# Optimization experiments

Hardware: AMD Instinct MI355X
Metric: run time of the kernel (lower is better)

The kernel has to match this reference:

```python
import jax, jax.numpy as jnp
import numpy as np

B, N, D, H = 4, 2048, 1024, 16
HD = D // H
SCALE = D ** -0.5  # NOTE: original scales by dimension**-0.5 (not head_dim**-0.5)


def setup_inputs() -> dict:
    key = jax.random.key(0)
    k1, k2, k3 = jax.random.split(key, 3)
    x = jax.random.normal(k1, (B, N, D), dtype=jnp.float32)
    w_qkv = jax.random.normal(k2, (D, 3 * D), dtype=jnp.float32) * (D ** -0.5)
    w_proj = jax.random.normal(k3, (D, D), dtype=jnp.float32) * (D ** -0.5)
    b_proj = jnp.zeros((D,), dtype=jnp.float32)
    return {"x": x, "w_qkv": w_qkv, "w_proj": w_proj, "b_proj": b_proj}


def reference(x, w_qkv, w_proj, b_proj):
    # qkv projection: [B,N,3D] -> split into q,k,v each [B,H,N,HD]
    qkv = x @ w_qkv
    qkv = qkv.reshape(B, N, 3, H, HD).transpose(2, 0, 3, 1, 4)  # [3,B,H,N,HD]
    q, k, v = qkv[0], qkv[1], qkv[2]
    scores = jnp.einsum('bhid,bhjd->bhij', q, k) * SCALE
    attn = jax.nn.softmax(scores, axis=-1)
    out = jnp.einsum('bhij,bhjd->bhid', attn, v)  # [B,H,N,HD]
    out = out.transpose(0, 2, 1, 3).reshape(B, N, D)
    return out @ w_proj + b_proj
```

## Files before the change

kernel.cpp:

```cpp
#include <hip/hip_runtime.h>
#include <stdint.h>

#define Bdim 4
#define Nseq 2048
#define Dmod 1024
#define Hn   16
#define HD   64
#define SCALE 0.03125f
#define L2E   1.44269504089f

typedef __attribute__((ext_vector_type(8))) short short8;
typedef __attribute__((ext_vector_type(8))) unsigned short ushort8;
typedef __attribute__((ext_vector_type(4))) float f32x4;
typedef __attribute__((ext_vector_type(16))) float f32x16;

typedef __attribute__((address_space(3))) uint32_t lds_u32;
typedef __attribute__((address_space(1))) const uint32_t glob_u32;

static __device__ __forceinline__ void gload_lds16(const unsigned short* g, unsigned short* l) {
    __builtin_amdgcn_global_load_lds((glob_u32*)(const void*)g, (lds_u32*)(void*)l, 16, 0, 0);
}

static __device__ __forceinline__ unsigned short f2bf(float f) {
    union { float f; uint32_t u; } v; v.f = f;
    uint32_t r = (v.u + 0x7FFFu + ((v.u >> 16) & 1u)) >> 16;
    return (unsigned short)r;
}

__global__ __launch_bounds__(256) void prep_kernel(const float* __restrict__ x,
                                                   const float* __restrict__ w_qkv,
                                                   const float* __restrict__ w_proj,
                                                   unsigned short* __restrict__ xb,
                                                   unsigned short* __restrict__ wqkvT,
                                                   unsigned short* __restrict__ wprojT) {
    __shared__ unsigned short t[32][33];
    int bid = blockIdx.x, tid = threadIdx.x;
    if (bid < 2048) {
        const int n4 = (Bdim * Nseq * Dmod) / 4;
        int i = bid * 256 + tid;
        for (; i < n4; i += 2048 * 256) {
            float4 v = reinterpret_cast<const float4*>(x)[i];
            ushort4 o;
            o.x = f2bf(v.x); o.y = f2bf(v.y); o.z = f2bf(v.z); o.w = f2bf(v.w);
            reinterpret_cast<ushort4*>(xb)[i] = o;
        }
        return;
    }
    const float* in;
    unsigned short* out;
    int R, C, c0, r0;
    if (bid < 5120) {
        int lin = bid - 2048;
        in = w_qkv; out = wqkvT; R = 1024; C = 3072;
        c0 = (lin % 96) * 32; r0 = (lin / 96) * 32;
    } else {
        int lin = bid - 5120;
        in = w_proj; out = wprojT; R = 1024; C = 1024;
        c0 = (lin % 32) * 32; r0 = (lin / 32) * 32;
    }
    int tx = tid & 31, ty = tid >> 5;
#pragma unroll
    for (int i = 0; i < 4; ++i)
        t[ty + i*8][tx] = f2bf(in[(size_t)(r0 + ty + i*8) * C + c0 + tx]);
    __syncthreads();
#pragma unroll
    for (int i = 0; i < 4; ++i)
        out[(size_t)(c0 + ty + i*8) * R + r0 + tx] = t[tx][ty + i*8];
}

template<bool OUT_BF16, bool BIAS, bool VSPLIT>
__global__ __launch_bounds__(256) void gemm_bt_kernel(const unsigned short* __restrict__ A,
                                                      const unsigned short* __restrict__ Bt,
                                                      void* __restrict__ Cv,
                                                      const float* __restrict__ bias,
                                                      unsigned short* __restrict__ vTp,
                                                      int M, int N, int K) {
    __shared__ unsigned short Al[128 * 64];
    __shared__ unsigned short Bl[128 * 64];
    int tid = threadIdx.x;
    int lane = tid & 63, wv = tid >> 6;
    int wr = (wv >> 1) * 64, wc = (wv & 1) * 64;
    int lr = lane & 15, lg = lane >> 4, lk = lg * 8;

    int gx = gridDim.x;
    int lin = blockIdx.y * gx + blockIdx.x;
    int cpx = (gx * gridDim.y) >> 3;
    int nl = (lin & 7) * cpx + (lin >> 3);
    int m0 = (nl / gx) * 128, n0 = (nl % gx) * 128;

    int srow = wv * 8 + (lane >> 3);
    int scol = (lane & 7) * 8;
    const unsigned short* ag = A  + (size_t)(m0 + srow) * K + scol;
    const unsigned short* bg = Bt + (size_t)(n0 + srow) * K + scol;
    unsigned short* la = Al + wv * 512;
    unsigned short* lb = Bl + wv * 512;

    f32x4 acc[4][4];
#pragma unroll
    for (int i = 0; i < 4; ++i)
#pragma unroll
        for (int j = 0; j < 4; ++j) acc[i][j] = (f32x4)0.f;

    for (int k0 = 0; k0 < K; k0 += 64) {
        __syncthreads();
#pragma unroll
        for (int i = 0; i < 4; ++i) {
            gload_lds16(ag + (size_t)i * 32 * K + k0, la + i * 2048);
            gload_lds16(bg + (size_t)i * 32 * K + k0, lb + i * 2048);
        }
        __syncthreads();
#pragma unroll
        for (int ks = 0; ks < 2; ++ks) {
            short8 a[4], b[4];
#pragma unroll
            for (int mi = 0; mi < 4; ++mi)
                a[mi] = *reinterpret_cast<const short8*>(Al + (wr + mi*16 + lr) * 64 + ks*32 + lk);
#pragma unroll
            for (int nj = 0; nj < 4; ++nj)
                b[nj] = *reinterpret_cast<const short8*>(Bl + (wc + nj*16 + lr) * 64 + ks*32 + lk);
#pragma unroll
            for (int mi = 0; mi < 4; ++mi)
#pragma unroll
                for (int nj = 0; nj < 4; ++nj)
                    acc[mi][nj] = __builtin_amdgcn_mfma_f32_16x16x32_bf16(a[mi], b[nj], acc[mi][nj], 0, 0, 0);
        }
    }
#pragma unroll
    for (int mi = 0; mi < 4; ++mi) {
#pragma unroll
        for (int nj = 0; nj < 4; ++nj) {
            int r = m0 + wr + mi*16 + lg*4;
            int c = n0 + wc + nj*16 + lr;
            if (VSPLIT && c >= 2048) {
                int cc = c - 2048;
                int bh = ((r >> 11) << 4) + (cc >> 6);
                int d = cc & 63;
                ushort4 o4;
                o4.x = f2bf(acc[mi][nj][0]);
                o4.y = f2bf(acc[mi][nj][1]);
                o4.z = f2bf(acc[mi][nj][2]);
                o4.w = f2bf(acc[mi][nj][3]);
                *reinterpret_cast<ushort4*>(vTp + ((size_t)(bh * 64 + d) * 2048) + (r & 2047)) = o4;
            } else {
                float bv = BIAS ? bias[c] : 0.f;
#pragma unroll
                for (int i = 0; i < 4; ++i) {
                    float v = acc[mi][nj][i] + bv;
                    if (OUT_BF16)
                        reinterpret_cast<unsigned short*>(Cv)[(size_t)(r + i) * N + c] = f2bf(v);
                    else
                        reinterpret_cast<float*>(Cv)[(size_t)(r + i) * N + c] = v;
                }
            }
        }
    }
}

__global__ __launch_bounds__(256, 2) void attn_kernel(const unsigned short* __restrict__ qkv,
                                                      const unsigned short* __restrict__ vT,
                                                      unsigned short* __restrict__ attn_o) {
    __shared__ unsigned short Kl[2 * 64 * 64];
    __shared__ unsigned short Vl[2 * 64 * 64];
    __shared__ unsigned short Pl[4 * 64 * 64];

    int w = blockIdx.x;
    int lid = (w & 7) * 64 + (w >> 3);
    int bh = lid >> 3, qb = lid & 7;
    int b = bh >> 4, h = bh & 15;

    int tid = threadIdx.x, lane = tid & 63, wv = tid >> 6;
    int lr = lane & 31, hi = lane >> 5;
    int q0 = qb * 256 + wv * 64;

    short8 qfA[4], qfB[4];
    {
        const unsigned short* qrowA = qkv + (size_t)(b * Nseq + q0 + lr) * 3072 + h * 64 + hi * 8;
        const unsigned short* qrowB = qrowA + (size_t)32 * 3072;
#pragma unroll
        for (int ks = 0; ks < 4; ++ks) {
            qfA[ks] = *reinterpret_cast<const short8*>(qrowA + ks * 16);
            qfB[ks] = *reinterpret_cast<const short8*>(qrowB + ks * 16);
        }
    }

    float mrunA = -1e30f, lrunA = 0.f, mrunB = -1e30f, lrunB = 0.f;
    f32x16 oA0 = (f32x16)0.f, oA1 = (f32x16)0.f, oB0 = (f32x16)0.f, oB1 = (f32x16)0.f;

    int sr = tid >> 2;
    const unsigned short* kg = qkv + (size_t)(b * Nseq + sr) * 3072 + 1024 + h * 64 + (tid & 3) * 16;
    const unsigned short* vg = vT + ((size_t)(bh * 64 + sr)) * Nseq + (tid & 3) * 16;
    int sb = (sr >> 5) * 4096 + (tid & 3) * 1024 + (sr & 31) * 16;
    char* Pw = (char*)Pl + wv * 8192 + lr * 16 + 8 * hi;
    char* Pr = (char*)Pl + wv * 8192 + lane * 16;

    {
        ushort8 a0 = *reinterpret_cast<const ushort8*>(kg);
        ushort8 a1 = *reinterpret_cast<const ushort8*>(kg + 8);
        ushort8 a2 = *reinterpret_cast<const ushort8*>(vg);
        ushort8 a3 = *reinterpret_cast<const ushort8*>(vg + 8);
        *reinterpret_cast<ushort8*>((char*)Kl + sb) = a0;
        *reinterpret_cast<ushort8*>((char*)Kl + sb + 512) = a1;
        *reinterpret_cast<ushort8*>((char*)Vl + sb) = a2;
        *reinterpret_cast<ushort8*>((char*)Vl + sb + 512) = a3;
    }
    ushort8 k0r = *reinterpret_cast<const ushort8*>(kg + (size_t)64 * 3072);
    ushort8 k1r = *reinterpret_cast<const ushort8*>(kg + (size_t)64 * 3072 + 8);
    ushort8 v0r = *reinterpret_cast<const ushort8*>(vg + 64);
    ushort8 v1r = *reinterpret_cast<const ushort8*>(vg + 72);

    int cur = 0;
    for (int jt = 0; jt < Nseq; jt += 64, cur ^= 1) {
        __syncthreads();
        int rb = cur * 8192, wb = rb ^ 8192;

        f32x16 sA0 = (f32x16)0.f, sA1 = (f32x16)0.f, sB0 = (f32x16)0.f, sB1 = (f32x16)0.f;
        __builtin_amdgcn_s_setprio(1);
#pragma unroll
        for (int ks = 0; ks < 4; ++ks) {
            short8 kf0 = *reinterpret_cast<const short8*>((char*)Kl + rb + ks*1024 + lane*16);
            short8 kf1 = *reinterpret_cast<const short8*>((char*)Kl + rb + 4096 + ks*1024 + lane*16);
            sA0 = __builtin_amdgcn_mfma_f32_32x32x16_bf16(kf0, qfA[ks], sA0, 0, 0, 0);
            sA1 = __builtin_amdgcn_mfma_f32_32x32x16_bf16(kf1, qfA[ks], sA1, 0, 0, 0);
            sB0 = __builtin_amdgcn_mfma_f32_32x32x16_bf16(kf0, qfB[ks], sB0, 0, 0, 0);
            sB1 = __builtin_amdgcn_mfma_f32_32x32x16_bf16(kf1, qfB[ks], sB1, 0, 0, 0);
        }
        __builtin_amdgcn_s_setprio(0);

        if (jt + 64 < Nseq) {
            *reinterpret_cast<ushort8*>((char*)Kl + wb + sb) = k0r;
            *reinterpret_cast<ushort8*>((char*)Kl + wb + sb + 512) = k1r;
            *reinterpret_cast<ushort8*>((char*)Vl + wb + sb) = v0r;
            *reinterpret_cast<ushort8*>((char*)Vl + wb + sb + 512) = v1r;
            int jn = jt + 128;
            if (jn < Nseq) {
                k0r = *reinterpret_cast<const ushort8*>(kg + (size_t)jn * 3072);
                k1r = *reinterpret_cast<const ushort8*>(kg + (size_t)jn * 3072 + 8);
                v0r = *reinterpret_cast<const ushort8*>(vg + jn);
                v1r = *reinterpret_cast<const ushort8*>(vg + jn + 8);
            }
        }

        float tA[16], tB[16];
#pragma unroll
        for (int i = 0; i < 16; ++i) { tA[i] = fmaxf(sA0[i], sA1[i]); tB[i] = fmaxf(sB0[i], sB1[i]); }
#pragma unroll
        for (int st = 8; st > 0; st >>= 1)
#pragma unroll
            for (int i = 0; i < st; ++i) { tA[i] = fmaxf(tA[i], tA[i + st]); tB[i] = fmaxf(tB[i], tB[i + st]); }
        float mlocA = fmaxf(tA[0], __shfl_xor(tA[0], 32)) * SCALE;
        float mlocB = fmaxf(tB[0], __shfl_xor(tB[0], 32)) * SCALE;

        if (!__all((mlocA <= mrunA + 8.f) && (mlocB <= mrunB + 8.f))) {
            float mnA = fmaxf(mrunA, mlocA);
            float fA = __builtin_amdgcn_exp2f((mrunA - mnA) * L2E);
            float mnB = fmaxf(mrunB, mlocB);
            float fB = __builtin_amdgcn_exp2f((mrunB - mnB) * L2E);
            lrunA *= fA; lrunB *= fB; mrunA = mnA; mrunB = mnB;
#pragma unroll
            for (int i = 0; i < 16; ++i) {
                oA0[i] *= fA; oA1[i] *= fA; oB0[i] *= fB; oB1[i] *= fB;
            }
        }

        const float c1 = SCALE * L2E;
        float c0A = -mrunA * L2E, c0B = -mrunB * L2E;
        float pA0[16], pA1[16], pB0[16], pB1[16];
#pragma unroll
        for (int i = 0; i < 16; ++i) {
            pA0[i] = __builtin_amdgcn_exp2f(fmaf(sA0[i], c1, c0A));
            pA1[i] = __builtin_amdgcn_exp2f(fmaf(sA1[i], c1, c0A));
            pB0[i] = __builtin_amdgcn_exp2f(fmaf(sB0[i], c1, c0B));
            pB1[i] = __builtin_amdgcn_exp2f(fmaf(sB1[i], c1, c0B));
        }

        uint32_t WA[16], WB[16];
#pragma unroll
        for (int m = 0; m < 8; ++m) {
            asm("v_cvt_pk_bf16_f32 %0, %1, %2" : "=v"(WA[m])   : "v"(pA0[2*m]), "v"(pA0[2*m+1]));
            asm("v_cvt_pk_bf16_f32 %0, %1, %2" : "=v"(WA[8+m]) : "v"(pA1[2*m]), "v"(pA1[2*m+1]));
            asm("v_cvt_pk_bf16_f32 %0, %1, %2" : "=v"(WB[m])   : "v"(pB0[2*m]), "v"(pB0[2*m+1]));
            asm("v_cvt_pk_bf16_f32 %0, %1, %2" : "=v"(WB[8+m]) : "v"(pB1[2*m]), "v"(pB1[2*m+1]));
        }
#pragma unroll
        for (int tt = 0; tt < 8; ++tt) {
            uint64_t valA = (uint64_t)WA[2*tt] | ((uint64_t)WA[2*tt+1] << 32);
            uint64_t valB = (uint64_t)WB[2*tt] | ((uint64_t)WB[2*tt+1] << 32);
            char* pa = Pw + (tt >> 1) * 1024 + (tt & 1) * 512;
            *reinterpret_cast<uint64_t*>(pa) = valA;
            *reinterpret_cast<uint64_t*>(pa + 4096) = valB;
        }

        float aA[16], aB[16];
#pragma unroll
        for (int i = 0; i < 16; ++i) { aA[i] = pA0[i] + pA1[i]; aB[i] = pB0[i] + pB1[i]; }
#pragma unroll
        for (int st = 8; st > 0; st >>= 1)
#pragma unroll
            for (int i = 0; i < st; ++i) { aA[i] += aA[i + st]; aB[i] += aB[i + st]; }
        lrunA += aA[0] + __shfl_xor(aA[0], 32);
        lrunB += aB[0] + __shfl_xor(aB[0], 32);

        __builtin_amdgcn_s_setprio(1);
#pragma unroll
        for (int ks4 = 0; ks4 < 4; ++ks4) {
            short8 vf0 = *reinterpret_cast<const short8*>((char*)Vl + rb + ks4*1024 + lane*16);
            short8 vf1 = *reinterpret_cast<const short8*>((char*)Vl + rb + 4096 + ks4*1024 + lane*16);
            short8 pfA = *reinterpret_cast<const short8*>(Pr + ks4*1024);
            short8 pfB = *reinterpret_cast<const short8*>(Pr + 4096 + ks4*1024);
            oA0 = __builtin_amdgcn_mfma_f32_32x32x16_bf16(vf0, pfA, oA0, 0, 0, 0);
            oA1 = __builtin_amdgcn_mfma_f32_32x32x16_bf16(vf1, pfA, oA1, 0, 0, 0);
            oB0 = __builtin_amdgcn_mfma_f32_32x32x16_bf16(vf0, pfB, oB0, 0, 0, 0);
            oB1 = __builtin_amdgcn_mfma_f32_32x32x16_bf16(vf1, pfB, oB1, 0, 0, 0);
        }
        __builtin_amdgcn_s_setprio(0);
    }

    float invA = 1.f / lrunA, invB = 1.f / lrunB;
    unsigned short* orowA = attn_o + (size_t)(b * Nseq + q0 + lr) * Dmod + h * 64;
    unsigned short* orowB = attn_o + (size_t)(b * Nseq + q0 + 32 + lr) * Dmod + h * 64;
#pragma unroll
    for (int db = 0; db < 2; ++db)
#pragma unroll
        for (int g = 0; g < 4; ++g) {
            int d = db * 32 + 8 * g + 4 * hi;
            ushort4 o4;
            o4.x = f2bf((db ? oA1[4*g+0] : oA0[4*g+0]) * invA);
            o4.y = f2bf((db ? oA1[4*g+1] : oA0[4*g+1]) * invA);
            o4.z = f2bf((db ? oA1[4*g+2] : oA0[4*g+2]) * invA);
            o4.w = f2bf((db ? oA1[4*g+3] : oA0[4*g+3]) * invA);
            *reinterpret_cast<ushort4*>(orowA + d) = o4;
            o4.x = f2bf((db ? oB1[4*g+0] : oB0[4*g+0]) * invB);
            o4.y = f2bf((db ? oB1[4*g+1] : oB0[4*g+1]) * invB);
            o4.z = f2bf((db ? oB1[4*g+2] : oB0[4*g+2]) * invB);
            o4.w = f2bf((db ? oB1[4*g+3] : oB0[4*g+3]) * invB);
            *reinterpret_cast<ushort4*>(orowB + d) = o4;
        }
}

extern "C" void kernel_launch(void* const* d_in, const int* in_sizes, int n_in,
                              void* d_out, int out_size, void* d_ws, size_t ws_size,
                              hipStream_t stream) {
    const float* x      = (const float*)d_in[0];
    const float* w_qkv  = (const float*)d_in[1];
    const float* w_proj = (const float*)d_in[2];
    const float* b_proj = (const float*)d_in[3];
    float* out = (float*)d_out;
    char* ws = (char*)d_ws;

    unsigned short* qkv    = (unsigned short*)(ws);
    unsigned short* vT     = (unsigned short*)(ws + 50331648);
    unsigned short* xb     = (unsigned short*)(ws + 67108864);
    unsigned short* attn_o = xb;
    unsigned short* wqkvT  = (unsigned short*)(ws + 83886080);
    unsigned short* wprojT = (unsigned short*)(ws + 90177536);

    prep_kernel<<<6144, 256, 0, stream>>>(x, w_qkv, w_proj, xb, wqkvT, wprojT);
    gemm_bt_kernel<true, false, true><<<dim3(3072/128, 8192/128), 256, 0, stream>>>(
        xb, wqkvT, qkv, nullptr, vT, Bdim*Nseq, 3*Dmod, Dmod);
    attn_kernel<<<512, 256, 0, stream>>>(qkv, vT, attn_o);
    gemm_bt_kernel<false, true, false><<<dim3(1024/128, 8192/128), 256, 0, stream>>>(
        attn_o, wprojT, out, b_proj, nullptr, Bdim*Nseq, Dmod, Dmod);
}
```

Before: 220.6 us.

## Add 256x256-tile double-buffered QKV GEMM with direct-to-LDS loads

Replaces the 128x128-tile QKV projection GEMM with a dedicated 512-thread kernel that computes 256x256 output tiles. It double-buffers A/B tiles in LDS using global_load_lds in an MFMA-fragment-native layout, prefetches the next K slice while computing, and raises wave priority around the MFMA bursts. The aim is more reuse per loaded byte and memory latency hidden behind compute. In exchange it uses 128KB of LDS per block, and its 384 blocks fill the CUs unevenly. The V-transpose epilogue moves into the new kernel, and the generic GEMM loses its VSPLIT path.

```diff
diff --git a/kernel.cpp b/kernel.cpp
--- a/kernel.cpp
+++ b/kernel.cpp
@@ -68,12 +68,123 @@
         out[(size_t)(c0 + ty + i*8) * R + r0 + tx] = t[tx][ty + i*8];
 }
 
-template<bool OUT_BF16, bool BIAS, bool VSPLIT>
+__global__ __launch_bounds__(512, 2) void gemm256_kernel(const unsigned short* __restrict__ A,
+                                                         const unsigned short* __restrict__ Bt,
+                                                         unsigned short* __restrict__ Cv,
+                                                         unsigned short* __restrict__ vTp) {
+    const int K = 1024, N = 3072;
+    __shared__ unsigned short Abuf[2 * 16384];
+    __shared__ unsigned short Bbuf[2 * 16384];
+
+    int tid = threadIdx.x;
+    int lane = tid & 63, w = tid >> 6;
+    int lr = lane & 15, lg = lane >> 4;
+
+    int lin = blockIdx.x;
+    int nl = (lin & 7) * 48 + (lin >> 3);
+    int m0 = (nl / 12) * 256, n0 = (nl % 12) * 256;
+
+    int wr = (w >> 2) * 128, wc = (w & 3) * 64;
+    int miG0 = wr >> 4, niG0 = wc >> 4;
+
+    const unsigned short* aSrc = A  + (size_t)(m0 + w*16 + lr) * K + lg * 8;
+    const unsigned short* bSrc = Bt + (size_t)(n0 + w*16 + lr) * K + lg * 8;
+
+    f32x4 acc[8][4];
+#pragma unroll
+    for (int i = 0; i < 8; ++i)
+#pragma unroll
+        for (int j = 0; j < 4; ++j) acc[i][j] = (f32x4)0.f;
+
+#pragma unroll
+    for (int h = 0; h < 2; ++h)
+#pragma unroll
+        for (int li = 0; li < 2; ++li) {
+            gload_lds16(aSrc + (size_t)h*128*K + li*32, Abuf + h*8192 + (w*2 + li)*512);
+            gload_lds16(bSrc + (size_t)h*128*K + li*32, Bbuf + h*8192 + (w*2 + li)*512);
+        }
+    asm volatile("s_waitcnt vmcnt(0)" ::: "memory");
+    __builtin_amdgcn_s_barrier();
+
+    for (int t = 0; t < 16; ++t) {
+        const char* Ab = (const char*)Abuf + (t & 1) * 32768;
+        const char* Bb = (const char*)Bbuf + (t & 1) * 32768;
+#pragma unroll
+        for (int q = 0; q < 4; ++q) {
+            const int mhb = (q >> 1) * 4, nhb = (q & 1) * 2;
+            short8 af[4][2], bf[2][2];
+#pragma unroll
+            for (int m2 = 0; m2 < 4; ++m2)
+#pragma unroll
+                for (int kk = 0; kk < 2; ++kk)
+                    af[m2][kk] = *reinterpret_cast<const short8*>(
+                        Ab + ((miG0 + mhb + m2) * 2 + kk) * 1024 + lane * 16);
+#pragma unroll
+            for (int n2 = 0; n2 < 2; ++n2)
+#pragma unroll
+                for (int kk = 0; kk < 2; ++kk)
+                    bf[n2][kk] = *reinterpret_cast<const short8*>(
+                        Bb + ((niG0 + nhb + n2) * 2 + kk) * 1024 + lane * 16);
+            if (q == 0 && t < 15) {
+                unsigned short* Ad = Abuf + ((t + 1) & 1) * 16384;
+                unsigned short* Bd = Bbuf + ((t + 1) & 1) * 16384;
+                const unsigned short* as = aSrc + (size_t)(t + 1) * 64;
+                const unsigned short* bs = bSrc + (size_t)(t + 1) * 64;
+#pragma unroll
+                for (int h = 0; h < 2; ++h)
+#pragma unroll
+                    for (int li = 0; li < 2; ++li) {
+                        gload_lds16(as + (size_t)h*128*K + li*32, Ad + h*8192 + (w*2 + li)*512);
+                        gload_lds16(bs + (size_t)h*128*K + li*32, Bd + h*8192 + (w*2 + li)*512);
+                    }
+            }
+            __builtin_amdgcn_s_barrier();
+            __builtin_amdgcn_s_setprio(1);
+#pragma unroll
+            for (int m2 = 0; m2 < 4; ++m2)
+#pragma unroll
+                for (int n2 = 0; n2 < 2; ++n2)
+#pragma unroll
+                    for (int kk = 0; kk < 2; ++kk)
+                        acc[mhb + m2][nhb + n2] = __builtin_amdgcn_mfma_f32_16x16x32_bf16(
+                            af[m2][kk], bf[n2][kk], acc[mhb + m2][nhb + n2], 0, 0, 0);
+            __builtin_amdgcn_s_setprio(0);
+            __builtin_amdgcn_s_barrier();
+        }
+        asm volatile("s_waitcnt vmcnt(0)" ::: "memory");
+        __builtin_amdgcn_s_barrier();
+    }
+
+#pragma unroll
+    for (int mi = 0; mi < 8; ++mi) {
+#pragma unroll
+        for (int ni = 0; ni < 4; ++ni) {
+            int r = m0 + wr + mi*16 + lg*4;
+            int c = n0 + wc + ni*16 + lr;
+            if (c >= 2048) {
+                int cc = c - 2048;
+                int bh = ((r >> 11) << 4) + (cc >> 6);
+                int d = cc & 63;
+                ushort4 o4;
+                o4.x = f2bf(acc[mi][ni][0]);
+                o4.y = f2bf(acc[mi][ni][1]);
+                o4.z = f2bf(acc[mi][ni][2]);
+                o4.w = f2bf(acc[mi][ni][3]);
+                *reinterpret_cast<ushort4*>(vTp + ((size_t)(bh * 64 + d) * 2048) + (r & 2047)) = o4;
+            } else {
+#pragma unroll
+                for (int i = 0; i < 4; ++i)
+                    Cv[(size_t)(r + i) * N + c] = f2bf(acc[mi][ni][i]);
+            }
+        }
+    }
+}
+
+template<bool OUT_BF16, bool BIAS>
 __global__ __launch_bounds__(256) void gemm_bt_kernel(const unsigned short* __restrict__ A,
                                                       const unsigned short* __restrict__ Bt,
                                                       void* __restrict__ Cv,
                                                       const float* __restrict__ bias,
-                                                      unsigned short* __restrict__ vTp,
                                                       int M, int N, int K) {
     __shared__ unsigned short Al[128 * 64];
     __shared__ unsigned short Bl[128 * 64];
@@ -131,26 +242,14 @@
         for (int nj = 0; nj < 4; ++nj) {
             int r = m0 + wr + mi*16 + lg*4;
             int c = n0 + wc + nj*16 + lr;
-            if (VSPLIT && c >= 2048) {
-                int cc = c - 2048;
-                int bh = ((r >> 11) << 4) + (cc >> 6);
-                int d = cc & 63;
-                ushort4 o4;
-                o4.x = f2bf(acc[mi][nj][0]);
-                o4.y = f2bf(acc[mi][nj][1]);
-                o4.z = f2bf(acc[mi][nj][2]);
-                o4.w = f2bf(acc[mi][nj][3]);
-                *reinterpret_cast<ushort4*>(vTp + ((size_t)(bh * 64 + d) * 2048) + (r & 2047)) = o4;
-            } else {
-                float bv = BIAS ? bias[c] : 0.f;
-#pragma unroll
-                for (int i = 0; i < 4; ++i) {
-                    float v = acc[mi][nj][i] + bv;
-                    if (OUT_BF16)
-                        reinterpret_cast<unsigned short*>(Cv)[(size_t)(r + i) * N + c] = f2bf(v);
-                    else
-                        reinterpret_cast<float*>(Cv)[(size_t)(r + i) * N + c] = v;
-                }
+            float bv = BIAS ? bias[c] : 0.f;
+#pragma unroll
+            for (int i = 0; i < 4; ++i) {
+                float v = acc[mi][nj][i] + bv;
+                if (OUT_BF16)
+                    reinterpret_cast<unsigned short*>(Cv)[(size_t)(r + i) * N + c] = f2bf(v);
+                else
+                    reinterpret_cast<float*>(Cv)[(size_t)(r + i) * N + c] = v;
             }
         }
     }
@@ -355,9 +454,8 @@
     unsigned short* wprojT = (unsigned short*)(ws + 90177536);
 
     prep_kernel<<<6144, 256, 0, stream>>>(x, w_qkv, w_proj, xb, wqkvT, wprojT);
-    gemm_bt_kernel<true, false, true><<<dim3(3072/128, 8192/128), 256, 0, stream>>>(
-        xb, wqkvT, qkv, nullptr, vT, Bdim*Nseq, 3*Dmod, Dmod);
+    gemm256_kernel<<<384, 512, 0, stream>>>(xb, wqkvT, qkv, vT);
     attn_kernel<<<512, 256, 0, stream>>>(qkv, vT, attn_o);
-    gemm_bt_kernel<false, true, false><<<dim3(1024/128, 8192/128), 256, 0, stream>>>(
-        attn_o, wprojT, out, b_proj, nullptr, Bdim*Nseq, Dmod, Dmod);
-}
+    gemm_bt_kernel<false, true><<<dim3(1024/128, 8192/128), 256, 0, stream>>>(
+        attn_o, wprojT, out, b_proj, Bdim*Nseq, Dmod, Dmod);
+}
```

Measured after the change: 254.9 us. 15.5% more time.

## Double-buffer GEMM with 256x128 tiles, 512 threads and fragment-major LDS layout

Applied to the files above, without the earlier changes.

Replaces the 128x128 single-buffered GEMM with a 256x128 tile kernel using 8 waves and double-buffered LDS, prefetching the next K slice while MFMAs run on the current one. LDS is laid out in MFMA fragment order so each lane reads contiguous 16 bytes, and s_setprio raises priority around the MFMA burst. The aim is to hide global-load latency and cut the barrier count per K step, at the cost of more LDS (96KB per block) and fewer blocks in flight.

```diff
diff --git a/kernel.cpp b/kernel.cpp
--- a/kernel.cpp
+++ b/kernel.cpp
@@ -69,31 +69,43 @@
 }
 
 template<bool OUT_BF16, bool BIAS, bool VSPLIT>
-__global__ __launch_bounds__(256) void gemm_bt_kernel(const unsigned short* __restrict__ A,
-                                                      const unsigned short* __restrict__ Bt,
-                                                      void* __restrict__ Cv,
-                                                      const float* __restrict__ bias,
-                                                      unsigned short* __restrict__ vTp,
-                                                      int M, int N, int K) {
-    __shared__ unsigned short Al[128 * 64];
-    __shared__ unsigned short Bl[128 * 64];
+__global__ __launch_bounds__(512, 2) void gemm_big_kernel(const unsigned short* __restrict__ A,
+                                                          const unsigned short* __restrict__ Bt,
+                                                          void* __restrict__ Cv,
+                                                          const float* __restrict__ bias,
+                                                          unsigned short* __restrict__ vTp,
+                                                          int N, int GX) {
+    const int K = 1024;
+    __shared__ unsigned short Abuf[2 * 16384];
+    __shared__ unsigned short Bbuf[2 * 8192];
+
     int tid = threadIdx.x;
-    int lane = tid & 63, wv = tid >> 6;
-    int wr = (wv >> 1) * 64, wc = (wv & 1) * 64;
-    int lr = lane & 15, lg = lane >> 4, lk = lg * 8;
-
-    int gx = gridDim.x;
-    int lin = blockIdx.y * gx + blockIdx.x;
-    int cpx = (gx * gridDim.y) >> 3;
+    int lane = tid & 63, w = tid >> 6;
+    int lr = lane & 15, lg = lane >> 4;
+
+    int lin = blockIdx.x;
+    int cpx = gridDim.x >> 3;
     int nl = (lin & 7) * cpx + (lin >> 3);
-    int m0 = (nl / gx) * 128, n0 = (nl % gx) * 128;
-
-    int srow = wv * 8 + (lane >> 3);
-    int scol = (lane & 7) * 8;
-    const unsigned short* ag = A  + (size_t)(m0 + srow) * K + scol;
-    const unsigned short* bg = Bt + (size_t)(n0 + srow) * K + scol;
-    unsigned short* la = Al + wv * 512;
-    unsigned short* lb = Bl + wv * 512;
+    int m0 = (nl / GX) * 256, n0 = (nl % GX) * 128;
+
+    int wr = (w >> 1) * 64, wc = (w & 1) * 64;
+    int miA0 = (wr >> 4), miB0 = (wc >> 4);
+
+    const unsigned short* aS[4];
+    unsigned short* aD[4];
+#pragma unroll
+    for (int j = 0; j < 4; ++j) {
+        int mi = w * 2 + (j >> 1), kk = j & 1;
+        aS[j] = A + (size_t)(m0 + mi * 16 + lr) * K + kk * 32 + lg * 8;
+        aD[j] = Abuf + (w * 4 + j) * 512;
+    }
+    const unsigned short* bS[2];
+    unsigned short* bD[2];
+#pragma unroll
+    for (int j = 0; j < 2; ++j) {
+        bS[j] = Bt + (size_t)(n0 + w * 16 + lr) * K + j * 32 + lg * 8;
+        bD[j] = Bbuf + (w * 2 + j) * 512;
+    }
 
     f32x4 acc[4][4];
 #pragma unroll
@@ -101,51 +113,71 @@
 #pragma unroll
         for (int j = 0; j < 4; ++j) acc[i][j] = (f32x4)0.f;
 
-    for (int k0 = 0; k0 < K; k0 += 64) {
-        __syncthreads();
-#pragma unroll
-        for (int i = 0; i < 4; ++i) {
-            gload_lds16(ag + (size_t)i * 32 * K + k0, la + i * 2048);
-            gload_lds16(bg + (size_t)i * 32 * K + k0, lb + i * 2048);
-        }
-        __syncthreads();
-#pragma unroll
-        for (int ks = 0; ks < 2; ++ks) {
-            short8 a[4], b[4];
-#pragma unroll
-            for (int mi = 0; mi < 4; ++mi)
-                a[mi] = *reinterpret_cast<const short8*>(Al + (wr + mi*16 + lr) * 64 + ks*32 + lk);
-#pragma unroll
-            for (int nj = 0; nj < 4; ++nj)
-                b[nj] = *reinterpret_cast<const short8*>(Bl + (wc + nj*16 + lr) * 64 + ks*32 + lk);
-#pragma unroll
-            for (int mi = 0; mi < 4; ++mi)
-#pragma unroll
-                for (int nj = 0; nj < 4; ++nj)
-                    acc[mi][nj] = __builtin_amdgcn_mfma_f32_16x16x32_bf16(a[mi], b[nj], acc[mi][nj], 0, 0, 0);
-        }
-    }
+#pragma unroll
+    for (int j = 0; j < 4; ++j) gload_lds16(aS[j], aD[j]);
+#pragma unroll
+    for (int j = 0; j < 2; ++j) gload_lds16(bS[j], bD[j]);
+    asm volatile("s_waitcnt vmcnt(0)" ::: "memory");
+    __builtin_amdgcn_s_barrier();
+
+    for (int t = 0; t < 16; ++t) {
+        if (t < 15) {
+            int bo = ((t + 1) & 1);
+#pragma unroll
+            for (int j = 0; j < 4; ++j) gload_lds16(aS[j] + (t + 1) * 64, aD[j] + bo * 16384);
+#pragma unroll
+            for (int j = 0; j < 2; ++j) gload_lds16(bS[j] + (t + 1) * 64, bD[j] + bo * 8192);
+        }
+        const char* Ab = (const char*)Abuf + (t & 1) * 32768;
+        const char* Bb = (const char*)Bbuf + (t & 1) * 16384;
+        short8 af[4][2], bf[4][2];
+#pragma unroll
+        for (int mi = 0; mi < 4; ++mi)
+#pragma unroll
+            for (int kk = 0; kk < 2; ++kk)
+                af[mi][kk] = *reinterpret_cast<const short8*>(
+                    Ab + ((miA0 + mi) * 2 + kk) * 1024 + lane * 16);
+#pragma unroll
+        for (int ni = 0; ni < 4; ++ni)
+#pragma unroll
+            for (int kk = 0; kk < 2; ++kk)
+                bf[ni][kk] = *reinterpret_cast<const short8*>(
+                    Bb + ((miB0 + ni) * 2 + kk) * 1024 + lane * 16);
+        __builtin_amdgcn_s_setprio(1);
+#pragma unroll
+        for (int mi = 0; mi < 4; ++mi)
+#pragma unroll
+            for (int ni = 0; ni < 4; ++ni)
+#pragma unroll
+                for (int kk = 0; kk < 2; ++kk)
+                    acc[mi][ni] = __builtin_amdgcn_mfma_f32_16x16x32_bf16(
+                        af[mi][kk], bf[ni][kk], acc[mi][ni], 0, 0, 0);
+        __builtin_amdgcn_s_setprio(0);
+        asm volatile("s_waitcnt vmcnt(0)" ::: "memory");
+        __builtin_amdgcn_s_barrier();
+    }
+
 #pragma unroll
     for (int mi = 0; mi < 4; ++mi) {
 #pragma unroll
-        for (int nj = 0; nj < 4; ++nj) {
+        for (int ni = 0; ni < 4; ++ni) {
             int r = m0 + wr + mi*16 + lg*4;
-            int c = n0 + wc + nj*16 + lr;
+            int c = n0 + wc + ni*16 + lr;
             if (VSPLIT && c >= 2048) {
                 int cc = c - 2048;
                 int bh = ((r >> 11) << 4) + (cc >> 6);
                 int d = cc & 63;
                 ushort4 o4;
-                o4.x = f2bf(acc[mi][nj][0]);
-                o4.y = f2bf(acc[mi][nj][1]);
-                o4.z = f2bf(acc[mi][nj][2]);
-                o4.w = f2bf(acc[mi][nj][3]);
+                o4.x = f2bf(acc[mi][ni][0]);
+                o4.y = f2bf(acc[mi][ni][1]);
+                o4.z = f2bf(acc[mi][ni][2]);
+                o4.w = f2bf(acc[mi][ni][3]);
                 *reinterpret_cast<ushort4*>(vTp + ((size_t)(bh * 64 + d) * 2048) + (r & 2047)) = o4;
             } else {
                 float bv = BIAS ? bias[c] : 0.f;
 #pragma unroll
                 for (int i = 0; i < 4; ++i) {
-                    float v = acc[mi][nj][i] + bv;
+                    float v = acc[mi][ni][i] + bv;
                     if (OUT_BF16)
                         reinterpret_cast<unsigned short*>(Cv)[(size_t)(r + i) * N + c] = f2bf(v);
                     else
@@ -355,9 +387,9 @@
     unsigned short* wprojT = (unsigned short*)(ws + 90177536);
 
     prep_kernel<<<6144, 256, 0, stream>>>(x, w_qkv, w_proj, xb, wqkvT, wprojT);
-    gemm_bt_kernel<true, false, true><<<dim3(3072/128, 8192/128), 256, 0, stream>>>(
-        xb, wqkvT, qkv, nullptr, vT, Bdim*Nseq, 3*Dmod, Dmod);
+    gemm_big_kernel<true, false, true><<<768, 512, 0, stream>>>(
+        xb, wqkvT, qkv, nullptr, vT, 3072, 24);
     attn_kernel<<<512, 256, 0, stream>>>(qkv, vT, attn_o);
-    gemm_bt_kernel<false, true, false><<<dim3(1024/128, 8192/128), 256, 0, stream>>>(
-        attn_o, wprojT, out, b_proj, nullptr, Bdim*Nseq, Dmod, Dmod);
-}
+    gemm_big_kernel<false, true, false><<<256, 512, 0, stream>>>(
+        attn_o, wprojT, out, b_proj, nullptr, 1024, 8);
+}
```

New measurement: 250.9 us. 1.14x slower.
